# Performance work log

Hardware: AMD Instinct MI355X
Metric: run time of the kernel (lower is better)

The kernel has to match this reference:

```python
import jax, jax.numpy as jnp
import numpy as np

EMBED = 1024
HEADS = 16
B, T = 4, 2048


def setup_inputs() -> dict:
    key = jax.random.key(0)
    k1, k2, k3, k4, k5 = jax.random.split(key, 5)
    s_in = 1.0 / np.sqrt(EMBED)
    return {
        "x": jax.random.normal(k1, (B, T, EMBED), dtype=jnp.float32),
        "w_qkv": jax.random.uniform(k2, (3 * EMBED, EMBED), jnp.float32, -s_in, s_in),
        "b_qkv": jax.random.uniform(k3, (3 * EMBED,), jnp.float32, -s_in, s_in),
        "w_proj": jax.random.uniform(k4, (EMBED, EMBED), jnp.float32, -s_in, s_in),
        "b_proj": jax.random.uniform(k5, (EMBED,), jnp.float32, -s_in, s_in),
    }


def reference(x, w_qkv, b_qkv, w_proj, b_proj):
    Bz, Tz, C = x.shape
    nh = HEADS
    hs = C // nh
    qkv = jnp.einsum('btc,oc->bto', x, w_qkv) + b_qkv  # [B,T,3C]
    q, k, v = jnp.split(qkv, 3, axis=-1)
    # [B, nh, T, hs]
    q = q.reshape(Bz, Tz, nh, hs).transpose(0, 2, 1, 3)
    k = k.reshape(Bz, Tz, nh, hs).transpose(0, 2, 1, 3)
    v = v.reshape(Bz, Tz, nh, hs).transpose(0, 2, 1, 3)
    scale = 1.0 / np.sqrt(hs).astype(np.float32)
    att = jnp.einsum('bhqd,bhkd->bhqk', q, k) * scale
    causal_mask = jnp.tril(jnp.ones((Tz, Tz), dtype=bool))
    att = jnp.where(causal_mask[None, None], att, jnp.finfo(att.dtype).min)
    att = jax.nn.softmax(att, axis=-1)
    y = jnp.einsum('bhqk,bhkd->bhqd', att, v)
    y = y.transpose(0, 2, 1, 3).reshape(Bz, Tz, C)
    return jnp.einsum('btc,oc->bto', y, w_proj) + b_proj
```

## Files before the change

kernel.cpp:

```cpp
#include <hip/hip_runtime.h>

typedef __bf16 bf16x8 __attribute__((ext_vector_type(8)));
typedef float f32x4 __attribute__((ext_vector_type(4)));

#define DI __device__ __forceinline__

#define WAIT_VMCNT(N)                                        \
  do {                                                       \
    __builtin_amdgcn_sched_barrier(0);                       \
    asm volatile("s_waitcnt vmcnt(" #N ")" ::: "memory");    \
    __builtin_amdgcn_sched_barrier(0);                       \
  } while (0)

DI unsigned short f2bf(float f) {
  unsigned int u = __float_as_uint(f);
  u += 0x7FFFu + ((u >> 16) & 1u);
  return (unsigned short)(u >> 16);
}

DI unsigned cvt_pk_bf16(float a, float b) {
  unsigned r;
  asm("v_cvt_pk_bf16_f32 %0, %1, %2" : "=v"(r) : "v"(a), "v"(b));
  return r;
}

DI float exp2_fast(float x) {
  float r;
  asm("v_exp_f32 %0, %1" : "=v"(r) : "v"(x));
  return r;
}

DI void fence() { asm volatile("" ::: "memory"); }
DI void bar() { fence(); __builtin_amdgcn_s_barrier(); fence(); }

DI bf16x8 ld16(const void* p) {
  union { uint4 u; bf16x8 b; } c;
  c.u = *reinterpret_cast<const uint4*>(p);
  return c.b;
}

DI f32x4 mfma16(bf16x8 a, bf16x8 b, f32x4 c) {
  return __builtin_amdgcn_mfma_f32_16x16x32_bf16(a, b, c, 0, 0, 0);
}

DI void gload_lds16(const void* g, void* l) {
  __builtin_amdgcn_global_load_lds(
      (const __attribute__((address_space(1))) unsigned int*)g,
      (__attribute__((address_space(3))) unsigned int*)l, 16, 0, 0);
}

__global__ void cvt_all(const float* __restrict__ x, const float* __restrict__ wq,
                        const float* __restrict__ wp,
                        unsigned short* __restrict__ xb, unsigned short* __restrict__ wqb,
                        unsigned short* __restrict__ wpb) {
  int i = blockIdx.x * blockDim.x + threadIdx.x;
  const float* s;
  unsigned short* d;
  int off;
  if (i < 2097152) { s = x; d = xb; off = i; }
  else if (i < 2097152 + 786432) { s = wq; d = wqb; off = i - 2097152; }
  else { s = wp; d = wpb; off = i - (2097152 + 786432); }
  float4 v = reinterpret_cast<const float4*>(s)[off];
  uint2 o;
  o.x = cvt_pk_bf16(v.x, v.y);
  o.y = cvt_pk_bf16(v.z, v.w);
  reinterpret_cast<uint2*>(d)[off] = o;
}

template <int N, int MODE>
__global__ __launch_bounds__(256)
void gemm_bt(const unsigned short* __restrict__ A,
             const unsigned short* __restrict__ W,
             const float* __restrict__ bias,
             float* __restrict__ out,
             unsigned short* __restrict__ qo,
             unsigned short* __restrict__ ko,
             unsigned short* __restrict__ vo) {
  constexpr int K = 1024;
  __shared__ __align__(16) char smem[32768];
  char* Asm = smem;
  char* Bsm = smem + 16384;
  const int tid = threadIdx.x;
  const int ln = tid & 63;
  const int w  = tid >> 6;
  const int wm = w >> 1, wn = w & 1;
  const int g = ln >> 4, q = ln & 15;
  const int m0 = blockIdx.x * 128;
  const int n0 = blockIdx.y * 128;

  f32x4 acc[4][4] = {};

  for (int kt = 0; kt < K / 64; ++kt) {
    if (kt) bar();
#pragma unroll
    for (int i = 0; i < 4; ++i) {
      const int chunk = i * 4 + w;
      const int o = chunk * 1024 + ln * 16;
      const int row = o >> 7;
      const int colb = (o & 127) ^ ((row & 7) << 4);
      gload_lds16((const char*)A + ((size_t)(m0 + row) * K + kt * 64) * 2 + colb,
                  Asm + chunk * 1024);
      gload_lds16((const char*)W + ((size_t)(n0 + row) * K + kt * 64) * 2 + colb,
                  Bsm + chunk * 1024);
    }
    WAIT_VMCNT(0);
    bar();
#pragma unroll
    for (int ks = 0; ks < 2; ++ks) {
      bf16x8 av[4], bv[4];
#pragma unroll
      for (int mf = 0; mf < 4; ++mf) {
        const int row = wm * 64 + mf * 16 + q;
        av[mf] = ld16(Asm + ((row * 128 + ks * 64 + g * 16) ^ ((row & 7) << 4)));
      }
#pragma unroll
      for (int nf = 0; nf < 4; ++nf) {
        const int row = wn * 64 + nf * 16 + q;
        bv[nf] = ld16(Bsm + ((row * 128 + ks * 64 + g * 16) ^ ((row & 7) << 4)));
      }
#pragma unroll
      for (int mf = 0; mf < 4; ++mf)
#pragma unroll
        for (int nf = 0; nf < 4; ++nf)
          acc[mf][nf] = mfma16(av[mf], bv[nf], acc[mf][nf]);
    }
  }

#pragma unroll
  for (int nf = 0; nf < 4; ++nf) {
    const int col = n0 + wn * 64 + nf * 16 + q;
    const float bv = bias[col];
#pragma unroll
    for (int mf = 0; mf < 4; ++mf) {
      const int rbase = m0 + wm * 64 + mf * 16 + g * 4;
      if constexpr (MODE == 0) {
#pragma unroll
        for (int r = 0; r < 4; ++r)
          out[(size_t)(rbase + r) * N + col] = acc[mf][nf][r] + bv;
      } else {
        const int b = rbase >> 11, t0 = rbase & 2047;
        if (col < 1024) {
          const int h = col >> 6, d = col & 63;
          unsigned short* qp = qo + ((((size_t)b * 16 + h) << 11) + t0) * 64 + d;
#pragma unroll
          for (int r = 0; r < 4; ++r)
            qp[r * 64] = f2bf((acc[mf][nf][r] + bv) * 0.18033688011112042f);
        } else if (col < 2048) {
          const int c = col - 1024;
          const int h = c >> 6, d = c & 63;
          unsigned short* kp = ko + ((((size_t)b * 16 + h) << 11) + t0) * 64 + d;
#pragma unroll
          for (int r = 0; r < 4; ++r)
            kp[r * 64] = f2bf(acc[mf][nf][r] + bv);
        } else {
          const int c = col - 2048;
          const int h = c >> 6, d = c & 63;
          uint2 pk;
          pk.x = cvt_pk_bf16(acc[mf][nf][0] + bv, acc[mf][nf][1] + bv);
          pk.y = cvt_pk_bf16(acc[mf][nf][2] + bv, acc[mf][nf][3] + bv);
          *(uint2*)(vo + ((((size_t)b * 16 + h) << 6) + d) * 2048 + t0) = pk;
        }
      }
    }
  }
}

__global__ __launch_bounds__(256, 4)
void attn_fwd(const unsigned short* __restrict__ Qb,
              const unsigned short* __restrict__ Kb,
              const unsigned short* __restrict__ Vtb,
              unsigned short* __restrict__ Yb) {
  __shared__ __align__(16) char smem[40960];
  const int tid = threadIdx.x;
  const int ln = tid & 63;
  const int w = tid >> 6;
  const int g = ln >> 4, q = ln & 15;
  char* Psm = smem + 32768 + w * 2048;
  const int bh = blockIdx.x;
  const int pair = blockIdx.y;
  const size_t base = (size_t)bh * 2048 * 64;
  const int b = bh >> 4, h = bh & 15;

  auto stage = [&](int j, int buf) {
    char* Kd = smem + buf * 16384;
    char* Vd = Kd + 8192;
    const int kv0 = j << 6;
    const char* Kg = (const char*)(Kb + base + (size_t)kv0 * 64);
    const char* Vg = (const char*)(Vtb + base) + kv0 * 2;
#pragma unroll
    for (int i = 0; i < 2; ++i) {
      const int chunk = i * 4 + w;
      const int o = chunk * 1024 + ln * 16;
      const int row = o >> 7;
      const int colb = (o & 127) ^ ((row & 7) << 4);
      gload_lds16(Kg + row * 128 + colb, Kd + chunk * 1024);
      gload_lds16(Vg + (size_t)row * 4096 + colb, Vd + chunk * 1024);
    }
  };

  auto run_qtile = [&](int qt) {
    const int q0 = qt * 64;
    const int qw = q0 + w * 16;

    bf16x8 qf[2];
#pragma unroll
    for (int kf = 0; kf < 2; ++kf)
      qf[kf] = ld16(Qb + base + (size_t)(qw + q) * 64 + kf * 32 + g * 8);
    WAIT_VMCNT(0);

    float m_run = -INFINITY;
    float l_run = 0.f;
    f32x4 yt[4] = {};

    const int nkv = qt + 1;
    stage(0, 0);
    for (int j = 0; j < nkv; ++j) {
      if (j + 1 < nkv) {
        stage(j + 1, (j + 1) & 1);
        WAIT_VMCNT(4);
      } else {
        WAIT_VMCNT(0);
      }
      bar();

      const int kv0 = j << 6;
      const char* Ksm = smem + (j & 1) * 16384;
      const char* Vsm = Ksm + 8192;
      f32x4 st[4] = {};
      __builtin_amdgcn_s_setprio(1);
#pragma unroll
      for (int mf = 0; mf < 4; ++mf) {
        const int row = mf * 16 + q;
        const int swz = (row & 7) << 4;
        const bf16x8 a0 = ld16(Ksm + ((row * 128 + g * 16) ^ swz));
        const bf16x8 a1 = ld16(Ksm + ((row * 128 + 64 + g * 16) ^ swz));
        st[mf] = mfma16(a0, qf[0], st[mf]);
        st[mf] = mfma16(a1, qf[1], st[mf]);
      }
      __builtin_amdgcn_s_setprio(0);
      if (kv0 + 63 > qw) {
#pragma unroll
        for (int mf = 0; mf < 4; ++mf)
#pragma unroll
          for (int r = 0; r < 4; ++r)
            if (kv0 + mf * 16 + g * 4 + r > qw + q)
              st[mf][r] = -INFINITY;
      }
      {
        float vmax = -INFINITY;
#pragma unroll
        for (int mf = 0; mf < 4; ++mf) {
          const f32x4 v = st[mf];
          vmax = fmaxf(fmaxf(vmax, fmaxf(v[0], v[1])), fmaxf(v[2], v[3]));
        }
        vmax = fmaxf(vmax, __shfl_xor(vmax, 16));
        vmax = fmaxf(vmax, __shfl_xor(vmax, 32));
        const float mo = m_run;
        if (__any(vmax > mo)) {
          const float mn = fmaxf(mo, vmax);
          const float corr = exp2_fast(mo - mn);
          m_run = mn;
          l_run *= corr;
#pragma unroll
          for (int mfd = 0; mfd < 4; ++mfd) yt[mfd] *= corr;
        }
        const float mcur = m_run;
        float ls = 0.f;
#pragma unroll
        for (int mf = 0; mf < 4; ++mf) {
          f32x4 p;
#pragma unroll
          for (int r = 0; r < 4; ++r) p[r] = exp2_fast(st[mf][r] - mcur);
          ls += (p[0] + p[1]) + (p[2] + p[3]);
          uint2 pk2;
          pk2.x = cvt_pk_bf16(p[0], p[1]);
          pk2.y = cvt_pk_bf16(p[2], p[3]);
          *(uint2*)(Psm + ((q * 128 + mf * 32 + g * 8) ^ ((q & 7) << 4))) = pk2;
        }
        ls += __shfl_xor(ls, 16);
        ls += __shfl_xor(ls, 32);
        l_run += ls;
      }
      asm volatile("s_waitcnt lgkmcnt(0)" ::: "memory");
      __builtin_amdgcn_sched_barrier(0);
      __builtin_amdgcn_s_setprio(1);
#pragma unroll
      for (int kf = 0; kf < 2; ++kf) {
        const bf16x8 pb = ld16(Psm + ((q * 128 + kf * 64 + g * 16) ^ ((q & 7) << 4)));
#pragma unroll
        for (int mfd = 0; mfd < 4; ++mfd) {
          const int vrow = mfd * 16 + q;
          const bf16x8 vv = ld16(Vsm + ((vrow * 128 + kf * 64 + g * 16) ^ ((vrow & 7) << 4)));
          yt[mfd] = mfma16(vv, pb, yt[mfd]);
        }
      }
      __builtin_amdgcn_s_setprio(0);
      bar();
    }

    const float inv = 1.f / l_run;
    const int qr = qw + q;
    unsigned short* yp = Yb + (size_t)(b * 2048 + qr) * 1024 + h * 64;
#pragma unroll
    for (int mfd = 0; mfd < 4; ++mfd) {
      uint2 o2;
      o2.x = cvt_pk_bf16(yt[mfd][0] * inv, yt[mfd][1] * inv);
      o2.y = cvt_pk_bf16(yt[mfd][2] * inv, yt[mfd][3] * inv);
      *(uint2*)(yp + mfd * 16 + g * 4) = o2;
    }
  };

  run_qtile(31 - pair);
  run_qtile(pair);
}

extern "C" void kernel_launch(void* const* d_in, const int* in_sizes, int n_in,
                              void* d_out, int out_size, void* d_ws, size_t ws_size,
                              hipStream_t stream) {
  const float* x      = (const float*)d_in[0];
  const float* w_qkv  = (const float*)d_in[1];
  const float* b_qkv  = (const float*)d_in[2];
  const float* w_proj = (const float*)d_in[3];
  const float* b_proj = (const float*)d_in[4];
  float* out = (float*)d_out;
  char* ws = (char*)d_ws;

  unsigned short* xb  = (unsigned short*)(ws);
  unsigned short* wqb = (unsigned short*)(ws + (size_t)(16 << 20));
  unsigned short* wpb = (unsigned short*)(ws + (size_t)(22 << 20));
  unsigned short* Qb  = (unsigned short*)(ws + (size_t)(24 << 20));
  unsigned short* Kb  = (unsigned short*)(ws + (size_t)(40 << 20));
  unsigned short* Vtb = (unsigned short*)(ws + (size_t)(56 << 20));
  unsigned short* Yb  = (unsigned short*)(ws + (size_t)(72 << 20));

  cvt_all<<<12288, 256, 0, stream>>>(x, w_qkv, w_proj, xb, wqb, wpb);
  gemm_bt<3072, 1><<<dim3(64, 24), 256, 0, stream>>>(xb, wqb, b_qkv, nullptr, Qb, Kb, Vtb);
  attn_fwd<<<dim3(64, 16), 256, 0, stream>>>(Qb, Kb, Vtb, Yb);
  gemm_bt<1024, 0><<<dim3(64, 8), 256, 0, stream>>>(Yb, wpb, b_proj, out, nullptr, nullptr, nullptr);
}
```

Before: 167.0 us.

## Keep softmax probabilities in registers by permuting K rows to match MFMA B layout

Reorders which K rows each MFMA fragment computes so the S accumulator layout directly matches the B-operand layout needed for the P·V MFMA. This removes the per-wave LDS round trip for P (stores, lgkmcnt wait, reloads) and shrinks shared memory from 40 KB to 32 KB. The causal mask indices are remapped to the new row permutation. It must keep the permutation consistent between the K rows, the mask and the V reduction ordering, or results will be wrong.

```diff
diff --git a/kernel.cpp b/kernel.cpp
--- a/kernel.cpp
+++ b/kernel.cpp
@@ -170,16 +170,16 @@
               const unsigned short* __restrict__ Kb,
               const unsigned short* __restrict__ Vtb,
               unsigned short* __restrict__ Yb) {
-  __shared__ __align__(16) char smem[40960];
+  __shared__ __align__(16) char smem[32768];
   const int tid = threadIdx.x;
   const int ln = tid & 63;
   const int w = tid >> 6;
   const int g = ln >> 4, q = ln & 15;
-  char* Psm = smem + 32768 + w * 2048;
   const int bh = blockIdx.x;
   const int pair = blockIdx.y;
   const size_t base = (size_t)bh * 2048 * 64;
   const int b = bh >> 4, h = bh & 15;
+  const int qrow = (q & 3) + 8 * (q >> 2);
 
   auto stage = [&](int j, int buf) {
     char* Kd = smem + buf * 16384;
@@ -229,28 +229,29 @@
       f32x4 st[4] = {};
       __builtin_amdgcn_s_setprio(1);
 #pragma unroll
-      for (int mf = 0; mf < 4; ++mf) {
-        const int row = mf * 16 + q;
+      for (int f = 0; f < 4; ++f) {
+        const int row = qrow + 4 * (f & 1) + 32 * (f >> 1);
         const int swz = (row & 7) << 4;
         const bf16x8 a0 = ld16(Ksm + ((row * 128 + g * 16) ^ swz));
         const bf16x8 a1 = ld16(Ksm + ((row * 128 + 64 + g * 16) ^ swz));
-        st[mf] = mfma16(a0, qf[0], st[mf]);
-        st[mf] = mfma16(a1, qf[1], st[mf]);
+        st[f] = mfma16(a0, qf[0], st[f]);
+        st[f] = mfma16(a1, qf[1], st[f]);
       }
       __builtin_amdgcn_s_setprio(0);
       if (kv0 + 63 > qw) {
 #pragma unroll
-        for (int mf = 0; mf < 4; ++mf)
+        for (int f = 0; f < 4; ++f) {
+          const int kvb = kv0 + 8 * g + 4 * (f & 1) + 32 * (f >> 1);
 #pragma unroll
           for (int r = 0; r < 4; ++r)
-            if (kv0 + mf * 16 + g * 4 + r > qw + q)
-              st[mf][r] = -INFINITY;
+            if (kvb + r > qw + q) st[f][r] = -INFINITY;
+        }
       }
       {
         float vmax = -INFINITY;
 #pragma unroll
-        for (int mf = 0; mf < 4; ++mf) {
-          const f32x4 v = st[mf];
+        for (int f = 0; f < 4; ++f) {
+          const f32x4 v = st[f];
           vmax = fmaxf(fmaxf(vmax, fmaxf(v[0], v[1])), fmaxf(v[2], v[3]));
         }
         vmax = fmaxf(vmax, __shfl_xor(vmax, 16));
@@ -267,32 +268,35 @@
         const float mcur = m_run;
         float ls = 0.f;
 #pragma unroll
-        for (int mf = 0; mf < 4; ++mf) {
-          f32x4 p;
-#pragma unroll
-          for (int r = 0; r < 4; ++r) p[r] = exp2_fast(st[mf][r] - mcur);
-          ls += (p[0] + p[1]) + (p[2] + p[3]);
-          uint2 pk2;
-          pk2.x = cvt_pk_bf16(p[0], p[1]);
-          pk2.y = cvt_pk_bf16(p[2], p[3]);
-          *(uint2*)(Psm + ((q * 128 + mf * 32 + g * 8) ^ ((q & 7) << 4))) = pk2;
+        for (int f = 0; f < 4; ++f) {
+#pragma unroll
+          for (int r = 0; r < 4; ++r) {
+            st[f][r] = exp2_fast(st[f][r] - mcur);
+            ls += st[f][r];
+          }
         }
         ls += __shfl_xor(ls, 16);
         ls += __shfl_xor(ls, 32);
         l_run += ls;
       }
-      asm volatile("s_waitcnt lgkmcnt(0)" ::: "memory");
-      __builtin_amdgcn_sched_barrier(0);
+      union { uint4 u; bf16x8 b; } pb0, pb1;
+      pb0.u.x = cvt_pk_bf16(st[0][0], st[0][1]);
+      pb0.u.y = cvt_pk_bf16(st[0][2], st[0][3]);
+      pb0.u.z = cvt_pk_bf16(st[1][0], st[1][1]);
+      pb0.u.w = cvt_pk_bf16(st[1][2], st[1][3]);
+      pb1.u.x = cvt_pk_bf16(st[2][0], st[2][1]);
+      pb1.u.y = cvt_pk_bf16(st[2][2], st[2][3]);
+      pb1.u.z = cvt_pk_bf16(st[3][0], st[3][1]);
+      pb1.u.w = cvt_pk_bf16(st[3][2], st[3][3]);
       __builtin_amdgcn_s_setprio(1);
 #pragma unroll
-      for (int kf = 0; kf < 2; ++kf) {
-        const bf16x8 pb = ld16(Psm + ((q * 128 + kf * 64 + g * 16) ^ ((q & 7) << 4)));
-#pragma unroll
-        for (int mfd = 0; mfd < 4; ++mfd) {
-          const int vrow = mfd * 16 + q;
-          const bf16x8 vv = ld16(Vsm + ((vrow * 128 + kf * 64 + g * 16) ^ ((vrow & 7) << 4)));
-          yt[mfd] = mfma16(vv, pb, yt[mfd]);
-        }
+      for (int mfd = 0; mfd < 4; ++mfd) {
+        const int vrow = mfd * 16 + q;
+        const int swz = (vrow & 7) << 4;
+        const bf16x8 v0 = ld16(Vsm + ((vrow * 128 + g * 16) ^ swz));
+        const bf16x8 v1 = ld16(Vsm + ((vrow * 128 + 64 + g * 16) ^ swz));
+        yt[mfd] = mfma16(v0, pb0.b, yt[mfd]);
+        yt[mfd] = mfma16(v1, pb1.b, yt[mfd]);
       }
       __builtin_amdgcn_s_setprio(0);
       bar();
```

After: 165.6 us. About the same (-0.9%).
